# Performance work log

Hardware: AMD Instinct MI355X
Metric: run time of the kernel (lower is better)

The kernel has to match this reference:

```python
import jax, jax.numpy as jnp
import numpy as np

B, S, H, E, TOP_K = 4, 2048, 1024, 16, 4


def setup_inputs() -> dict:
    key = jax.random.key(0)
    ks = jax.random.split(key, 12)
    sc = 1.0 / np.sqrt(H)
    inp = {
        "x": jax.random.normal(ks[0], (B, S, H), dtype=jnp.float32),
        "image": jax.random.normal(ks[1], (B, S, H), dtype=jnp.float32),
        "text": jax.random.normal(ks[2], (B, S, H), dtype=jnp.float32),
        "audio": jax.random.normal(ks[3], (B, S, H), dtype=jnp.float32),
        # generalized router linear
        "Wg": jax.random.uniform(ks[4], (H, E), jnp.float32, -sc, sc),
        "bg": jax.random.uniform(ks[5], (E,), jnp.float32, -sc, sc),
        # per-modality router linears
        "Wi": jax.random.uniform(ks[6], (H, E), jnp.float32, -sc, sc),
        "bi": jax.random.uniform(ks[7], (E,), jnp.float32, -sc, sc),
        "Wt": jax.random.uniform(ks[8], (H, E), jnp.float32, -sc, sc),
        "bt": jax.random.uniform(ks[9], (E,), jnp.float32, -sc, sc),
        "Wa": jax.random.uniform(ks[10], (H, E), jnp.float32, -sc, sc),
        "ba": jax.random.uniform(ks[11], (E,), jnp.float32, -sc, sc),
    }
    return inp


def reference(x, image, text, audio, Wg, bg, Wi, bi, Wt, bt, Wa, ba):
    # combined_logits = generalized_router(x) + sum_m modality_router_m(modality_m)
    logits = (
        jnp.einsum("bsh,he->bse", x, Wg) + bg
        + jnp.einsum("bsh,he->bse", image, Wi) + bi
        + jnp.einsum("bsh,he->bse", text, Wt) + bt
        + jnp.einsum("bsh,he->bse", audio, Wa) + ba
    )  # [B,S,E]
    router_probs = jax.nn.softmax(logits, axis=-1)
    top_k_probs, top_k_indices = jax.lax.top_k(router_probs, TOP_K)
    top_k_probs = top_k_probs / jnp.sum(top_k_probs, axis=-1, keepdims=True)
    prob_per_expert = jnp.mean(router_probs, axis=(0, 1))  # [E]
    aux_loss = jnp.sum(prob_per_expert * jnp.log(prob_per_expert * E + 1e-9))
    return (top_k_indices, top_k_probs, aux_loss)
```

## Files before the change

kernel.cpp:

```cpp
#include <hip/hip_runtime.h>
#include <math.h>

constexpr int kTokens = 8192;
constexpr int kH      = 1024;
constexpr int kE      = 16;
constexpr int kTopK   = 4;
constexpr int kNC     = 16;

__global__ __launch_bounds__(256, 3)
void router_fmac(const float* __restrict__ x,   const float* __restrict__ img,
                 const float* __restrict__ txt, const float* __restrict__ aud,
                 const float* __restrict__ Wg,  const float* __restrict__ Wi,
                 const float* __restrict__ Wt,  const float* __restrict__ Wa,
                 float* __restrict__ partials)
{
    __shared__ float wlds[4096];
    __shared__ float xlds[256 * 36];

    const int t   = threadIdx.x;
    const int w   = t >> 6;
    const int ln  = t & 63;
    const int tq  = ln >> 2;
    const int eq  = ln & 3;
    const int bid = blockIdx.x;
    const int ks  = bid >> 5;
    const int tg  = bid & 31;
    const int m   = ks >> 2;
    const int k0  = (ks & 3) * 256;
    const int tok0 = tg * 256;

    const float* Xm = (m == 0) ? x  : (m == 1) ? img : (m == 2) ? txt : aud;
    const float* Wm = (m == 0) ? Wg : (m == 1) ? Wi  : (m == 2) ? Wt  : Wa;

    {
        const float4* wsrc = (const float4*)(Wm + (size_t)k0 * kE);
#pragma unroll
        for (int i = 0; i < 4; ++i) {
            const float4 v = wsrc[t + i * 256];
            *(float4*)&wlds[(t + i * 256) * 4] = v;
        }
    }

    const int sc = t & 7;
    const int sr = t >> 3;
    float4 pf[8];

    {
        const float* src = Xm + (size_t)(tok0 + sr) * kH + k0 + sc * 4;
#pragma unroll
        for (int i = 0; i < 8; ++i)
            pf[i] = *(const float4*)(src + (size_t)(i * 32) * kH);
#pragma unroll
        for (int i = 0; i < 8; ++i)
            *(float4*)&xlds[(sr + i * 32) * 36 + sc * 4] = pf[i];
    }
    __syncthreads();

    float  facc[4][4];
    double dacc[4][4];
#pragma unroll
    for (int i = 0; i < 4; ++i)
#pragma unroll
        for (int q = 0; q < 4; ++q) dacc[i][q] = 0.0;

    const int r0 = w * 64 + tq;

    for (int p = 0; p < 8; ++p) {
        if (p < 7) {
            const float* src = Xm + (size_t)(tok0 + sr) * kH + k0 + (p + 1) * 32 + sc * 4;
#pragma unroll
            for (int i = 0; i < 8; ++i)
                pf[i] = *(const float4*)(src + (size_t)(i * 32) * kH);
        }

        if ((p & 1) == 0) {
#pragma unroll
            for (int i = 0; i < 4; ++i)
#pragma unroll
                for (int q = 0; q < 4; ++q) facc[i][q] = 0.f;
        }

#pragma unroll
        for (int h4 = 0; h4 < 8; ++h4) {
            float4 xv[4];
#pragma unroll
            for (int i = 0; i < 4; ++i)
                xv[i] = *(const float4*)&xlds[(r0 + 16 * i) * 36 + h4 * 4];
#pragma unroll
            for (int j = 0; j < 4; ++j) {
                const float4 wv = *(const float4*)&wlds[(p * 32 + h4 * 4 + j) * 16 + eq * 4];
#pragma unroll
                for (int i = 0; i < 4; ++i) {
                    const float xh = (j == 0) ? xv[i].x : (j == 1) ? xv[i].y
                                   : (j == 2) ? xv[i].z : xv[i].w;
                    facc[i][0] += xh * wv.x;  facc[i][1] += xh * wv.y;
                    facc[i][2] += xh * wv.z;  facc[i][3] += xh * wv.w;
                }
            }
        }

        if ((p & 1) == 1) {
#pragma unroll
            for (int i = 0; i < 4; ++i)
#pragma unroll
                for (int q = 0; q < 4; ++q) dacc[i][q] += (double)facc[i][q];
        }

        __syncthreads();
        if (p < 7) {
#pragma unroll
            for (int i = 0; i < 8; ++i)
                *(float4*)&xlds[(sr + i * 32) * 36 + sc * 4] = pf[i];
        }
        __syncthreads();
    }

#pragma unroll
    for (int i = 0; i < 4; ++i) {
        const int token = tok0 + w * 64 + tq + 16 * i;
        *(float4*)&partials[((size_t)ks * kTokens + token) * kE + eq * 4] =
            make_float4((float)dacc[i][0], (float)dacc[i][1],
                        (float)dacc[i][2], (float)dacc[i][3]);
    }
}

__global__ __launch_bounds__(256)
void router_topk(const float* __restrict__ partials,
                 const float* __restrict__ bg, const float* __restrict__ bi,
                 const float* __restrict__ bt, const float* __restrict__ ba,
                 float* __restrict__ out, float* __restrict__ blocksum)
{
    __shared__ double lgs[64][kE + 1];
    __shared__ float  pr[64][kE + 1];

    const int t    = threadIdx.x;
    const int tq   = t >> 2;
    const int eq   = t & 3;
    const int tok0 = blockIdx.x * 64;

    double a0 = (double)bg[eq*4+0] + (double)bi[eq*4+0] + (double)bt[eq*4+0] + (double)ba[eq*4+0];
    double a1 = (double)bg[eq*4+1] + (double)bi[eq*4+1] + (double)bt[eq*4+1] + (double)ba[eq*4+1];
    double a2 = (double)bg[eq*4+2] + (double)bi[eq*4+2] + (double)bt[eq*4+2] + (double)ba[eq*4+2];
    double a3 = (double)bg[eq*4+3] + (double)bi[eq*4+3] + (double)bt[eq*4+3] + (double)ba[eq*4+3];

#pragma unroll
    for (int c = 0; c < kNC; ++c) {
        const float4 v = *(const float4*)(partials + ((size_t)c * kTokens + tok0 + tq) * kE + eq * 4);
        a0 += (double)v.x;  a1 += (double)v.y;  a2 += (double)v.z;  a3 += (double)v.w;
    }
    lgs[tq][eq*4+0] = a0;  lgs[tq][eq*4+1] = a1;
    lgs[tq][eq*4+2] = a2;  lgs[tq][eq*4+3] = a3;
    __syncthreads();

    if (t < 64) {
        const int tok = tok0 + t;
        double lg[kE];
#pragma unroll
        for (int e = 0; e < kE; ++e) lg[e] = lgs[t][e];

        double mx = lg[0];
#pragma unroll
        for (int e = 1; e < kE; ++e) mx = fmax(mx, lg[e]);

        float p[kE];
        float sum = 0.f;
#pragma unroll
        for (int e = 0; e < kE; ++e) {
            p[e] = expf((float)(lg[e] - mx));
            sum += p[e];
        }
        const float inv = 1.f / sum;
#pragma unroll
        for (int e = 0; e < kE; ++e) { p[e] *= inv; pr[t][e] = p[e]; }

        unsigned used = 0;
        float tp[kTopK];
        int   ti[kTopK];
        float s4 = 0.f;
#pragma unroll
        for (int k = 0; k < kTopK; ++k) {
            float best = -1.f;
            int   bidx = 0;
#pragma unroll
            for (int e = 0; e < kE; ++e) {
                if (!((used >> e) & 1u) && p[e] > best) { best = p[e]; bidx = e; }
            }
            used |= 1u << bidx;
            tp[k] = best;
            ti[k] = bidx;
            s4 += best;
        }
        const float rn = 1.f / s4;

        *(float4*)&out[(size_t)tok * kTopK] =
            make_float4((float)ti[0], (float)ti[1], (float)ti[2], (float)ti[3]);
        *(float4*)&out[(size_t)kTokens * kTopK + (size_t)tok * kTopK] =
            make_float4(tp[0] * rn, tp[1] * rn, tp[2] * rn, tp[3] * rn);
    }
    __syncthreads();

    if (t < kE) {
        float s = 0.f;
#pragma unroll
        for (int tk = 0; tk < 64; ++tk) s += pr[tk][t];
        blocksum[blockIdx.x * kE + t] = s;
    }
}

__global__ __launch_bounds__(64)
void router_aux(const float* __restrict__ blocksum, float* __restrict__ out)
{
    __shared__ double ps[kE];
    const int t = threadIdx.x;
    if (t < kE) {
        double s = 0.0;
        for (int b = 0; b < 128; ++b) s += (double)blocksum[b * kE + t];
        ps[t] = s / (double)kTokens;
    }
    __syncthreads();
    if (t == 0) {
        double aux = 0.0;
#pragma unroll
        for (int e = 0; e < kE; ++e) aux += ps[e] * log(ps[e] * (double)kE + 1e-9);
        out[(size_t)kTokens * kTopK * 2] = (float)aux;
    }
}

extern "C" void kernel_launch(void* const* d_in, const int* in_sizes, int n_in,
                              void* d_out, int out_size, void* d_ws, size_t ws_size,
                              hipStream_t stream)
{
    const float* x   = (const float*)d_in[0];
    const float* img = (const float*)d_in[1];
    const float* txt = (const float*)d_in[2];
    const float* aud = (const float*)d_in[3];
    const float* Wg  = (const float*)d_in[4];
    const float* bg  = (const float*)d_in[5];
    const float* Wi  = (const float*)d_in[6];
    const float* bi  = (const float*)d_in[7];
    const float* Wt  = (const float*)d_in[8];
    const float* bt  = (const float*)d_in[9];
    const float* Wa  = (const float*)d_in[10];
    const float* ba  = (const float*)d_in[11];

    float* out      = (float*)d_out;
    float* partials = (float*)d_ws;
    float* blocksum = (float*)((char*)d_ws + (size_t)kNC * kTokens * kE * 4);

    router_fmac<<<512, 256, 0, stream>>>(x, img, txt, aud, Wg, Wi, Wt, Wa, partials);
    router_topk<<<128, 256, 0, stream>>>(partials, bg, bi, bt, ba, out, blocksum);
    router_aux<<<1, 64, 0, stream>>>(blocksum, out);
}
```

Before: 210.6 us.

## Split hidden dim into 32 chunks, double-buffer X tiles, read weights from global

```diff
diff --git a/kernel.cpp b/kernel.cpp
--- a/kernel.cpp
+++ b/kernel.cpp
@@ -5,17 +5,20 @@
 constexpr int kH      = 1024;
 constexpr int kE      = 16;
 constexpr int kTopK   = 4;
-constexpr int kNC     = 16;
-
-__global__ __launch_bounds__(256, 3)
+
+template<int NC>
+__global__ __launch_bounds__(256, 4)
 void router_fmac(const float* __restrict__ x,   const float* __restrict__ img,
                  const float* __restrict__ txt, const float* __restrict__ aud,
                  const float* __restrict__ Wg,  const float* __restrict__ Wi,
                  const float* __restrict__ Wt,  const float* __restrict__ Wa,
                  float* __restrict__ partials)
 {
-    __shared__ float wlds[4096];
-    __shared__ float xlds[256 * 36];
+    constexpr int KEXT = 4096 / NC;
+    constexpr int P    = KEXT / 16;
+    constexpr int MS   = NC / 4;
+
+    __shared__ float xt[2][256 * 20];
 
     const int t   = threadIdx.x;
     const int w   = t >> 6;
@@ -23,94 +26,74 @@
     const int tq  = ln >> 2;
     const int eq  = ln & 3;
     const int bid = blockIdx.x;
-    const int ks  = bid >> 5;
-    const int tg  = bid & 31;
-    const int m   = ks >> 2;
-    const int k0  = (ks & 3) * 256;
+    const int ks  = bid & (NC - 1);
+    const int tg  = bid / NC;
+    const int m   = ks / MS;
+    const int h0  = (ks % MS) * KEXT;
     const int tok0 = tg * 256;
 
     const float* Xm = (m == 0) ? x  : (m == 1) ? img : (m == 2) ? txt : aud;
     const float* Wm = (m == 0) ? Wg : (m == 1) ? Wi  : (m == 2) ? Wt  : Wa;
 
-    {
-        const float4* wsrc = (const float4*)(Wm + (size_t)k0 * kE);
-#pragma unroll
-        for (int i = 0; i < 4; ++i) {
-            const float4 v = wsrc[t + i * 256];
-            *(float4*)&wlds[(t + i * 256) * 4] = v;
-        }
-    }
-
-    const int sc = t & 7;
-    const int sr = t >> 3;
-    float4 pf[8];
-
-    {
-        const float* src = Xm + (size_t)(tok0 + sr) * kH + k0 + sc * 4;
-#pragma unroll
-        for (int i = 0; i < 8; ++i)
-            pf[i] = *(const float4*)(src + (size_t)(i * 32) * kH);
-#pragma unroll
-        for (int i = 0; i < 8; ++i)
-            *(float4*)&xlds[(sr + i * 32) * 36 + sc * 4] = pf[i];
-    }
-    __syncthreads();
-
-    float  facc[4][4];
-    double dacc[4][4];
+    const int sc = t & 3;
+    const int sr = t >> 2;
+    const float* gbase = Xm + (size_t)tok0 * kH + h0 + sc * 4;
+
+    float4 pf[4];
+
 #pragma unroll
     for (int i = 0; i < 4; ++i)
-#pragma unroll
-        for (int q = 0; q < 4; ++q) dacc[i][q] = 0.0;
+        pf[i] = *(const float4*)(gbase + (size_t)(sr + 64 * i) * kH);
+#pragma unroll
+    for (int i = 0; i < 4; ++i)
+        *(float4*)&xt[0][(sr + 64 * i) * 20 + sc * 4] = pf[i];
+    __syncthreads();
+
+    float facc[4][4];
+#pragma unroll
+    for (int i = 0; i < 4; ++i)
+#pragma unroll
+        for (int q = 0; q < 4; ++q) facc[i][q] = 0.f;
 
     const int r0 = w * 64 + tq;
 
-    for (int p = 0; p < 8; ++p) {
-        if (p < 7) {
-            const float* src = Xm + (size_t)(tok0 + sr) * kH + k0 + (p + 1) * 32 + sc * 4;
-#pragma unroll
-            for (int i = 0; i < 8; ++i)
-                pf[i] = *(const float4*)(src + (size_t)(i * 32) * kH);
-        }
-
-        if ((p & 1) == 0) {
+#pragma unroll
+    for (int p = 0; p < P; ++p) {
+        if (p < P - 1) {
 #pragma unroll
             for (int i = 0; i < 4; ++i)
-#pragma unroll
-                for (int q = 0; q < 4; ++q) facc[i][q] = 0.f;
-        }
-
-#pragma unroll
-        for (int h4 = 0; h4 < 8; ++h4) {
+                pf[i] = *(const float4*)(gbase + (size_t)(sr + 64 * i) * kH + (p + 1) * 16);
+        }
+
+        const float* buf = xt[p & 1];
+        const float* wp  = Wm + (size_t)(h0 + p * 16) * kE + eq * 4;
+
+#pragma unroll
+        for (int hg = 0; hg < 4; ++hg) {
+            float4 wv[4];
+#pragma unroll
+            for (int j = 0; j < 4; ++j)
+                wv[j] = *(const float4*)(wp + (hg * 4 + j) * kE);
             float4 xv[4];
 #pragma unroll
             for (int i = 0; i < 4; ++i)
-                xv[i] = *(const float4*)&xlds[(r0 + 16 * i) * 36 + h4 * 4];
+                xv[i] = *(const float4*)&buf[(r0 + 16 * i) * 20 + hg * 4];
 #pragma unroll
             for (int j = 0; j < 4; ++j) {
-                const float4 wv = *(const float4*)&wlds[(p * 32 + h4 * 4 + j) * 16 + eq * 4];
 #pragma unroll
                 for (int i = 0; i < 4; ++i) {
                     const float xh = (j == 0) ? xv[i].x : (j == 1) ? xv[i].y
                                    : (j == 2) ? xv[i].z : xv[i].w;
-                    facc[i][0] += xh * wv.x;  facc[i][1] += xh * wv.y;
-                    facc[i][2] += xh * wv.z;  facc[i][3] += xh * wv.w;
+                    facc[i][0] += xh * wv[j].x;  facc[i][1] += xh * wv[j].y;
+                    facc[i][2] += xh * wv[j].z;  facc[i][3] += xh * wv[j].w;
                 }
             }
         }
 
-        if ((p & 1) == 1) {
+        if (p < P - 1) {
 #pragma unroll
             for (int i = 0; i < 4; ++i)
-#pragma unroll
-                for (int q = 0; q < 4; ++q) dacc[i][q] += (double)facc[i][q];
-        }
-
-        __syncthreads();
-        if (p < 7) {
-#pragma unroll
-            for (int i = 0; i < 8; ++i)
-                *(float4*)&xlds[(sr + i * 32) * 36 + sc * 4] = pf[i];
+                *(float4*)&xt[(p + 1) & 1][(sr + 64 * i) * 20 + sc * 4] = pf[i];
         }
         __syncthreads();
     }
@@ -119,11 +102,11 @@
     for (int i = 0; i < 4; ++i) {
         const int token = tok0 + w * 64 + tq + 16 * i;
         *(float4*)&partials[((size_t)ks * kTokens + token) * kE + eq * 4] =
-            make_float4((float)dacc[i][0], (float)dacc[i][1],
-                        (float)dacc[i][2], (float)dacc[i][3]);
-    }
-}
-
+            make_float4(facc[i][0], facc[i][1], facc[i][2], facc[i][3]);
+    }
+}
+
+template<int NC>
 __global__ __launch_bounds__(256)
 void router_topk(const float* __restrict__ partials,
                  const float* __restrict__ bg, const float* __restrict__ bi,
@@ -144,7 +127,7 @@
     double a3 = (double)bg[eq*4+3] + (double)bi[eq*4+3] + (double)bt[eq*4+3] + (double)ba[eq*4+3];
 
 #pragma unroll
-    for (int c = 0; c < kNC; ++c) {
+    for (int c = 0; c < NC; ++c) {
         const float4 v = *(const float4*)(partials + ((size_t)c * kTokens + tok0 + tq) * kE + eq * 4);
         a0 += (double)v.x;  a1 += (double)v.y;  a2 += (double)v.z;  a3 += (double)v.w;
     }
@@ -243,11 +226,20 @@
     const float* Wa  = (const float*)d_in[10];
     const float* ba  = (const float*)d_in[11];
 
-    float* out      = (float*)d_out;
-    float* partials = (float*)d_ws;
-    float* blocksum = (float*)((char*)d_ws + (size_t)kNC * kTokens * kE * 4);
-
-    router_fmac<<<512, 256, 0, stream>>>(x, img, txt, aud, Wg, Wi, Wt, Wa, partials);
-    router_topk<<<128, 256, 0, stream>>>(partials, bg, bi, bt, ba, out, blocksum);
-    router_aux<<<1, 64, 0, stream>>>(blocksum, out);
-}
+    float* out = (float*)d_out;
+
+    const size_t need32 = (size_t)32 * kTokens * kE * 4 + 128 * kE * 4;
+    if (ws_size >= need32) {
+        float* partials = (float*)d_ws;
+        float* blocksum = (float*)((char*)d_ws + (size_t)32 * kTokens * kE * 4);
+        router_fmac<32><<<1024, 256, 0, stream>>>(x, img, txt, aud, Wg, Wi, Wt, Wa, partials);
+        router_topk<32><<<128, 256, 0, stream>>>(partials, bg, bi, bt, ba, out, blocksum);
+        router_aux<<<1, 64, 0, stream>>>(blocksum, out);
+    } else {
+        float* partials = (float*)d_ws;
+        float* blocksum = (float*)((char*)d_ws + (size_t)16 * kTokens * kE * 4);
+        router_fmac<16><<<512, 256, 0, stream>>>(x, img, txt, aud, Wg, Wi, Wt, Wa, partials);
+        router_topk<16><<<128, 256, 0, stream>>>(partials, bg, bi, bt, ba, out, blocksum);
+        router_aux<<<1, 64, 0, stream>>>(blocksum, out);
+    }
+}
```

Measured after the change: 211.7 us. No clear change (+0.6%).
